# Kernel tuning notes

Hardware: AMD Instinct MI355X
Metric: run time of the kernel (lower is better)

## Reference

```python
import jax, jax.numpy as jnp
import numpy as np


def setup_inputs() -> dict:
    key = jax.random.key(0)
    k1, k2 = jax.random.split(key)
    N = 8192
    similarity = jax.random.normal(k1, (N, N), dtype=jnp.float32)
    text_to_img_mapping = jax.random.randint(k2, (N,), 0, N, dtype=jnp.int64)
    return {"similarity": similarity, "text_to_img_mapping": text_to_img_mapping}


def reference(similarity, text_to_img_mapping):
    n_text, n_img = similarity.shape
    rows = jnp.arange(n_text)
    # text->image CE: mean over text rows of -log_softmax(sim, axis=1)[i, map[i]]
    lsm_rows = jax.nn.log_softmax(similarity, axis=1)
    text_loss = -jnp.mean(lsm_rows[rows, text_to_img_mapping])
    # image->text CE with multi-hot soft targets mask[img, txt] = 1 iff map[txt] == img.
    # -sum(mask * log_softmax(sim.T, axis=1)) / n_img
    #   == -sum_i log_softmax(sim, axis=0)[i, map[i]] / n_img  (gather, no NxN mask)
    lsm_cols = jax.nn.log_softmax(similarity, axis=0)
    visual_loss = -jnp.sum(lsm_cols[rows, text_to_img_mapping]) / n_img
    return (text_loss + visual_loss) / 2.0
```

## Files before the change

### kernel.cpp

```cpp
#include <hip/hip_runtime.h>
#include <hip/hip_bf16.h>
#include <math.h>

#define N 8192
#define RB 16
#define T1 512
#define NRC (N / RB)
#define CPT 16


__global__ __launch_bounds__(T1)
void stage1(const float* __restrict__ sim, const long long* __restrict__ map,
            float* __restrict__ colS,
            float* __restrict__ blkPart) {
    const int tid = threadIdx.x;
    const int rc = blockIdx.x;
    const int rowBase = rc * RB;

    float cs[CPT];
    #pragma unroll
    for (int k = 0; k < CPT; ++k) cs[k] = 0.f;

    __shared__ float lrow[RB][T1];
    __shared__ float rowLog[RB];

    float gsum = 0.f;

    #pragma unroll 2
    for (int r = 0; r < RB; ++r) {
        const int row = rowBase + r;
        const float4* p = (const float4*)(sim + (size_t)row * N);
        float4 v0 = p[tid];
        float4 v1 = p[tid + T1];
        float4 v2 = p[tid + 2 * T1];
        float4 v3 = p[tid + 3 * T1];

        if (tid == 0) {
            int c = (int)map[row];
            gsum += sim[(size_t)row * N + c];
        }

        float e0 = __expf(v0.x), e1 = __expf(v0.y), e2 = __expf(v0.z), e3 = __expf(v0.w);
        float e4 = __expf(v1.x), e5 = __expf(v1.y), e6 = __expf(v1.z), e7 = __expf(v1.w);
        float e8 = __expf(v2.x), e9 = __expf(v2.y), eA = __expf(v2.z), eB = __expf(v2.w);
        float eC = __expf(v3.x), eD = __expf(v3.y), eE = __expf(v3.z), eF = __expf(v3.w);

        cs[0] += e0; cs[1] += e1; cs[2]  += e2; cs[3]  += e3;
        cs[4] += e4; cs[5] += e5; cs[6]  += e6; cs[7]  += e7;
        cs[8] += e8; cs[9] += e9; cs[10] += eA; cs[11] += eB;
        cs[12] += eC; cs[13] += eD; cs[14] += eE; cs[15] += eF;

        float rp = (((e0 + e1) + (e2 + e3)) + ((e4 + e5) + (e6 + e7)))
                 + (((e8 + e9) + (eA + eB)) + ((eC + eD) + (eE + eF)));
        lrow[r][tid] = rp;
    }
    __syncthreads();

    {
        const int r = tid >> 5, j = tid & 31;
        float s = 0.f;
        #pragma unroll
        for (int k = 0; k < T1 / 32; ++k)
            s += lrow[r][j + 32 * k];
        s += __shfl_xor(s, 1);
        s += __shfl_xor(s, 2);
        s += __shfl_xor(s, 4);
        s += __shfl_xor(s, 8);
        s += __shfl_xor(s, 16);
        if (j == 0) rowLog[r] = __logf(s);
    }
    __syncthreads();

    if (tid == 0) {
        float b = -2.0f * gsum;
        #pragma unroll
        for (int r = 0; r < RB; ++r) b += rowLog[r];
        blkPart[rc] = b;
    }

    float4* outp = (float4*)(colS + (size_t)rc * N);
    outp[tid]          = make_float4(cs[0],  cs[1],  cs[2],  cs[3]);
    outp[tid + T1]     = make_float4(cs[4],  cs[5],  cs[6],  cs[7]);
    outp[tid + 2 * T1] = make_float4(cs[8],  cs[9],  cs[10], cs[11]);
    outp[tid + 3 * T1] = make_float4(cs[12], cs[13], cs[14], cs[15]);
}

__global__ __launch_bounds__(512)
void stage2(const float* __restrict__ colS, float* __restrict__ colLSE) {
    const int tid = threadIdx.x;
    const int cl = tid & 31;
    const int slice = tid >> 5;
    const int g = blockIdx.x * 32 + cl;

    float s = 0.f;
    #pragma unroll 4
    for (int k = 0; k < NRC / 16; ++k)
        s += colS[(size_t)(slice * (NRC / 16) + k) * N + g];

    __shared__ float lds[16][32];
    lds[slice][cl] = s;
    __syncthreads();

    if (tid < 32) {
        float t = 0.f;
        #pragma unroll
        for (int w = 0; w < 16; ++w) t += lds[w][tid];
        colLSE[blockIdx.x * 32 + tid] = __logf(t);
    }
}

__global__ __launch_bounds__(1024)
void stage3(const long long* __restrict__ map,
            const float* __restrict__ colLSE, const float* __restrict__ blkPart,
            float* __restrict__ out) {
    const int tid = threadIdx.x;
    float v = 0.f;
    if (tid < NRC) v = blkPart[tid];
    #pragma unroll
    for (int k = 0; k < N / 1024; ++k) {
        int i = k * 1024 + tid;
        v += colLSE[(int)map[i]];
    }
    #pragma unroll
    for (int off = 32; off >= 1; off >>= 1)
        v += __shfl_xor(v, off);
    __shared__ float red[16];
    const int wave = tid >> 6, lane = tid & 63;
    if (lane == 0) red[wave] = v;
    __syncthreads();
    if (tid == 0) {
        float t = 0.f;
        #pragma unroll
        for (int w = 0; w < 16; ++w) t += red[w];
        out[0] = t / (2.0f * (float)N);
    }
}

extern "C" void kernel_launch(void* const* d_in, const int* in_sizes, int n_in,
                              void* d_out, int out_size, void* d_ws, size_t ws_size,
                              hipStream_t stream) {
    const float* sim = (const float*)d_in[0];
    const long long* map = (const long long*)d_in[1];
    float* out = (float*)d_out;

    float* ws = (float*)d_ws;
    float* colS    = ws;
    float* colLSE  = colS + (size_t)NRC * N;
    float* blkPart = colLSE + N;

    stage1<<<NRC, T1, 0, stream>>>(sim, map, colS, blkPart);
    stage2<<<N / 32, 512, 0, stream>>>(colS, colLSE);
    stage3<<<1, 1024, 0, stream>>>(map, colLSE, blkPart, out);
}
```

Before: 58.19 us.

## Fold column-LSE gather into stage2 via per-block map histogram; double row block

Stage2 now builds a shared-memory histogram of how often each of its 32 columns appears in the mapping. It multiplies each column's log-sum-exp by that count and writes one partial per block. This removes the per-column LSE buffer and the 8192-element random gather in the single-block stage3, which now only sums 256 partials. Rows per stage1 block double to 32, which halves the column-partial buffer written and re-read. The trade-off is half as many stage1 blocks and twice the shared memory per block, which could lower occupancy on the bandwidth-bound main pass. Every stage2 block also scans the full map.

```diff
diff --git a/kernel.cpp b/kernel.cpp
--- a/kernel.cpp
+++ b/kernel.cpp
@@ -3,7 +3,7 @@
 #include <math.h>
 
 #define N 8192
-#define RB 16
+#define RB 32
 #define T1 512
 #define NRC (N / RB)
 #define CPT 16
@@ -57,16 +57,15 @@
     __syncthreads();
 
     {
-        const int r = tid >> 5, j = tid & 31;
+        const int r = tid >> 4, j = tid & 15;
         float s = 0.f;
         #pragma unroll
-        for (int k = 0; k < T1 / 32; ++k)
-            s += lrow[r][j + 32 * k];
+        for (int k = 0; k < T1 / 16; ++k)
+            s += lrow[r][j + 16 * k];
         s += __shfl_xor(s, 1);
         s += __shfl_xor(s, 2);
         s += __shfl_xor(s, 4);
         s += __shfl_xor(s, 8);
-        s += __shfl_xor(s, 16);
         if (j == 0) rowLog[r] = __logf(s);
     }
     __syncthreads();
@@ -86,11 +85,26 @@
 }
 
 __global__ __launch_bounds__(512)
-void stage2(const float* __restrict__ colS, float* __restrict__ colLSE) {
+void stage2(const float* __restrict__ colS, const long long* __restrict__ map,
+            float* __restrict__ colDot) {
     const int tid = threadIdx.x;
     const int cl = tid & 31;
     const int slice = tid >> 5;
-    const int g = blockIdx.x * 32 + cl;
+    const int colBase = blockIdx.x * 32;
+    const int g = colBase + cl;
+
+    __shared__ int cnt[32];
+    if (tid < 32) cnt[tid] = 0;
+    __syncthreads();
+
+    {
+        const long long* m = map;
+        #pragma unroll 4
+        for (int k = 0; k < N / 512; ++k) {
+            int c = (int)m[k * 512 + tid];
+            if ((c >> 5) == blockIdx.x) atomicAdd(&cnt[c & 31], 1);
+        }
+    }
 
     float s = 0.f;
     #pragma unroll 4
@@ -105,35 +119,30 @@
         float t = 0.f;
         #pragma unroll
         for (int w = 0; w < 16; ++w) t += lds[w][tid];
-        colLSE[blockIdx.x * 32 + tid] = __logf(t);
+        float v = (float)cnt[tid] * __logf(t);
+        v += __shfl_xor(v, 1);
+        v += __shfl_xor(v, 2);
+        v += __shfl_xor(v, 4);
+        v += __shfl_xor(v, 8);
+        v += __shfl_xor(v, 16);
+        if (tid == 0) colDot[blockIdx.x] = v;
     }
 }
 
-__global__ __launch_bounds__(1024)
-void stage3(const long long* __restrict__ map,
-            const float* __restrict__ colLSE, const float* __restrict__ blkPart,
+__global__ __launch_bounds__(256)
+void stage3(const float* __restrict__ blkPart, const float* __restrict__ colDot,
             float* __restrict__ out) {
     const int tid = threadIdx.x;
-    float v = 0.f;
-    if (tid < NRC) v = blkPart[tid];
-    #pragma unroll
-    for (int k = 0; k < N / 1024; ++k) {
-        int i = k * 1024 + tid;
-        v += colLSE[(int)map[i]];
-    }
+    float v = blkPart[tid] + colDot[tid];
     #pragma unroll
     for (int off = 32; off >= 1; off >>= 1)
         v += __shfl_xor(v, off);
-    __shared__ float red[16];
+    __shared__ float red[4];
     const int wave = tid >> 6, lane = tid & 63;
     if (lane == 0) red[wave] = v;
     __syncthreads();
-    if (tid == 0) {
-        float t = 0.f;
-        #pragma unroll
-        for (int w = 0; w < 16; ++w) t += red[w];
-        out[0] = t / (2.0f * (float)N);
-    }
+    if (tid == 0)
+        out[0] = (red[0] + red[1] + red[2] + red[3]) / (2.0f * (float)N);
 }
 
 extern "C" void kernel_launch(void* const* d_in, const int* in_sizes, int n_in,
@@ -145,10 +154,10 @@
 
     float* ws = (float*)d_ws;
     float* colS    = ws;
-    float* colLSE  = colS + (size_t)NRC * N;
-    float* blkPart = colLSE + N;
+    float* blkPart = colS + (size_t)NRC * N;
+    float* colDot  = blkPart + NRC;
 
     stage1<<<NRC, T1, 0, stream>>>(sim, map, colS, blkPart);
-    stage2<<<N / 32, 512, 0, stream>>>(colS, colLSE);
-    stage3<<<1, 1024, 0, stream>>>(map, colLSE, blkPart, out);
+    stage2<<<N / 32, 512, 0, stream>>>(colS, map, colDot);
+    stage3<<<1, 256, 0, stream>>>(blkPart, colDot, out);
 }
```

Result: faster. 55.49 us (-4.6%).
